# Kernel optimization log

Hardware: AMD Instinct MI355X
Metric: run time of the kernel (lower is better)

Reference implementation:

```python
import jax, jax.numpy as jnp
import numpy as np

B, T, E, V, H = 2, 2048, 1024, 2048, 8
KD, HD = E // H, V // H  # key_dim=128, head_dim=256
EPS = 1e-6


def rotate_every_two(x):
    x1 = x[..., ::2]
    x2 = x[..., 1::2]
    return jnp.stack((-x2, x1), axis=-1).reshape(x.shape)


def theta_shift(x, sin, cos):
    return x * cos + rotate_every_two(x) * sin


def setup_inputs() -> dict:
    key = jax.random.key(0)
    ks = jax.random.split(key, 8)
    x = jax.random.normal(ks[0], (B, T, E), dtype=jnp.float32)
    angle = jnp.arange(T, dtype=jnp.float32)[:, None] * (1.0 / (10000.0 ** (jnp.repeat(jnp.arange(KD // 2, dtype=jnp.float32), 2) * 2.0 / KD)))
    sin = jnp.sin(angle)  # [T, KD]
    cos = jnp.cos(angle)
    # RetNet per-head causal decay mask: decay_h = 1 - 2^(-5-h)
    decay = 1.0 - 2.0 ** (-5.0 - jnp.arange(H, dtype=jnp.float32))  # [H]
    idx = jnp.arange(T, dtype=jnp.float32)
    diff = idx[:, None] - idx[None, :]  # n - m
    causal = diff >= 0
    mask = jnp.where(causal[None], jnp.exp(jnp.where(causal, diff, 0.0)[None] * jnp.log(decay)[:, None, None]), 0.0)  # [H,T,T]
    g = 2 ** (-2.5)
    Wq = jax.random.normal(ks[1], (E, E), dtype=jnp.float32) * (g * np.sqrt(2.0 / (E + E)))
    Wk = jax.random.normal(ks[2], (E, E), dtype=jnp.float32) * (g * np.sqrt(2.0 / (E + E)))
    Wv = jax.random.normal(ks[3], (E, V), dtype=jnp.float32) * (g * np.sqrt(2.0 / (E + V)))
    Wg = jax.random.normal(ks[4], (E, V), dtype=jnp.float32) * (g * np.sqrt(2.0 / (E + V)))
    Wo = jax.random.normal(ks[5], (V, E), dtype=jnp.float32) * np.sqrt(2.0 / (V + E))
    return {"x": x, "sin": sin, "cos": cos, "mask": mask,
            "Wq": Wq, "Wk": Wk, "Wv": Wv, "Wg": Wg, "Wo": Wo}


def reference(x, sin, cos, mask, Wq, Wk, Wv, Wg, Wo):
    b, t, _ = x.shape
    scaling = KD ** -0.5
    q = (x @ Wq).reshape(b, t, H, KD).transpose(0, 2, 1, 3)  # [B,H,T,KD]
    k = (x @ Wk * scaling).reshape(b, t, H, KD).transpose(0, 2, 1, 3)
    v = x @ Wv  # [B,T,V]
    g = x @ Wg
    qr = theta_shift(q, sin, cos)
    kr = theta_shift(k, sin, cos)
    vr = v.reshape(b, t, H, HD).transpose(0, 2, 1, 3)  # [B,H,T,HD]
    qk = jnp.einsum('bhsk,bhtk->bhst', qr, kr) * mask  # [B,H,T,T]
    denom = jnp.clip(jnp.abs(jax.lax.stop_gradient(qk).sum(-1, keepdims=True)), 1.0, None)
    qk = qk / denom
    out = jnp.einsum('bhst,bhtd->bhsd', qk, vr)  # [B,H,T,HD]
    out = out.transpose(0, 2, 1, 3)  # [B,T,H,HD]
    # RMSNorm over head_dim, no affine
    out = out * jax.lax.rsqrt(jnp.mean(out * out, axis=-1, keepdims=True) + EPS)
    out = out.reshape(b, t, H * HD)
    out = jax.nn.silu(g) * out
    return out @ Wo  # [B,T,E]
```

## Files before the change

### kernel.cpp

```cpp
#include <hip/hip_runtime.h>
#include <hip/hip_bf16.h>


#define B_ 2
#define T_ 2048
#define E_ 1024
#define V_ 2048
#define H_ 8
#define KD_ 128
#define HD_ 256
#define M_ 4096

typedef __attribute__((ext_vector_type(8))) short bf16x8;
typedef __attribute__((ext_vector_type(4))) float f32x4;

__device__ __forceinline__ float u2f(unsigned short u) {
    return __uint_as_float(((unsigned)u) << 16);
}
__device__ __forceinline__ unsigned short f2bu(float f) {
    unsigned x = __float_as_uint(f);
    return (unsigned short)((x + 0x7fffu + ((x >> 16) & 1u)) >> 16);
}

typedef const __attribute__((address_space(1))) void gas_t;
typedef __attribute__((address_space(3))) void las_t;
__device__ __forceinline__ void gl_lds16(const void* g, void* l) {
    __builtin_amdgcn_global_load_lds((gas_t*)g, (las_t*)l, 16, 0, 0);
}

__global__ __launch_bounds__(256) void conv_x_kernel(
    const float* __restrict__ x, unsigned short* __restrict__ xb)
{
    const size_t i = ((size_t)blockIdx.x * 256 + threadIdx.x) * 8;
    float4 a = *(const float4*)(x + i);
    float4 c = *(const float4*)(x + i + 4);
    *(ushort4*)(xb + i)     = make_ushort4(f2bu(a.x), f2bu(a.y), f2bu(a.z), f2bu(a.w));
    *(ushort4*)(xb + i + 4) = make_ushort4(f2bu(c.x), f2bu(c.y), f2bu(c.z), f2bu(c.w));
}

__global__ __launch_bounds__(256) void transW5_kernel(
    const float* __restrict__ Wq, const float* __restrict__ Wk,
    const float* __restrict__ Wv, const float* __restrict__ Wg,
    const float* __restrict__ Wo,
    unsigned short* __restrict__ Wt, unsigned short* __restrict__ wot)
{
    const int z = blockIdx.z;
    const float* W; int N; int rofs; int Kd; unsigned short* dst;
    if (z == 0)      { W = Wq; N = 1024; rofs = 0;    Kd = 1024; dst = Wt; }
    else if (z == 1) { W = Wk; N = 1024; rofs = 1024; Kd = 1024; dst = Wt; }
    else if (z == 2) { W = Wv; N = 2048; rofs = 2048; Kd = 1024; dst = Wt; }
    else if (z == 3) { W = Wg; N = 2048; rofs = 4096; Kd = 1024; dst = Wt; }
    else             { W = Wo; N = 1024; rofs = 0;    Kd = 2048; dst = wot; }
    const int n0 = blockIdx.x * 64;
    const int k0 = blockIdx.y * 64;
    if (n0 >= N || k0 >= Kd) return;

    __shared__ float tl[64][65];
    const int tid = threadIdx.x;
    #pragma unroll
    for (int i = 0; i < 4; ++i) {
        int kr = i * 16 + (tid >> 4);
        int nc = (tid & 15) * 4;
        float4 v = *(const float4*)(W + (size_t)(k0 + kr) * N + n0 + nc);
        tl[kr][nc] = v.x; tl[kr][nc + 1] = v.y; tl[kr][nc + 2] = v.z; tl[kr][nc + 3] = v.w;
    }
    __syncthreads();
    #pragma unroll
    for (int i = 0; i < 4; ++i) {
        int nr = i * 16 + (tid >> 4);
        int kc = (tid & 15) * 4;
        ushort4 u = make_ushort4(f2bu(tl[kc + 0][nr]), f2bu(tl[kc + 1][nr]),
                                 f2bu(tl[kc + 2][nr]), f2bu(tl[kc + 3][nr]));
        *(ushort4*)(dst + (size_t)(rofs + n0 + nr) * Kd + k0 + kc) = u;
    }
}

__global__ __launch_bounds__(256) void transV_kernel(
    const unsigned short* __restrict__ vb, unsigned short* __restrict__ vt)
{
    __shared__ unsigned short tl[64][68];
    const int tid = threadIdx.x;
    const int t0 = blockIdx.x * 64, c0 = blockIdx.y * 64, b = blockIdx.z;
    #pragma unroll
    for (int i = 0; i < 4; ++i) {
        int tr = i * 16 + (tid >> 4);
        int cc = (tid & 15) * 4;
        ushort4 v = *(const ushort4*)(vb + (size_t)(b * T_ + t0 + tr) * V_ + c0 + cc);
        tl[tr][cc] = v.x; tl[tr][cc + 1] = v.y; tl[tr][cc + 2] = v.z; tl[tr][cc + 3] = v.w;
    }
    __syncthreads();
    #pragma unroll
    for (int i = 0; i < 4; ++i) {
        int cr = i * 16 + (tid >> 4);
        int tc = (tid & 15) * 4;
        ushort4 u = make_ushort4(tl[tc + 0][cr], tl[tc + 1][cr], tl[tc + 2][cr], tl[tc + 3][cr]);
        *(ushort4*)(vt + (size_t)(b * V_ + c0 + cr) * T_ + t0 + tc) = u;
    }
}

#define GSTAGE(BUF, K0)                                                        \
    {                                                                          \
        _Pragma("unroll")                                                      \
        for (int i = 0; i < 4; ++i) {                                          \
            int r = i * 32 + srow;                                             \
            int cb = scolb ^ ((r & 7) << 4);                                   \
            gl_lds16((const char*)(A  + (size_t)(rowBase + r) * K + (K0)) + cb,\
                     Asm[BUF] + i * 4096 + w * 1024);                          \
            gl_lds16((const char*)(Bt + (size_t)(colBase + r) * K + (K0)) + cb,\
                     Bsm[BUF] + i * 4096 + w * 1024);                          \
        }                                                                      \
    }

#define GCOMPUTE(BUF)                                                          \
    {                                                                          \
        _Pragma("unroll")                                                      \
        for (int kk = 0; kk < 2; ++kk) {                                       \
            const int cb = kk * 64 + (l >> 4) * 16;                            \
            bf16x8 a[4], b[4];                                                 \
            _Pragma("unroll")                                                  \
            for (int m = 0; m < 4; ++m) {                                      \
                int r = wr * 64 + m * 16 + (l & 15);                           \
                a[m] = *(const bf16x8*)(Asm[BUF] + r * 128 + (cb ^ ((r & 7) << 4))); \
            }                                                                  \
            _Pragma("unroll")                                                  \
            for (int n = 0; n < 4; ++n) {                                      \
                int r = wc * 64 + n * 16 + (l & 15);                           \
                b[n] = *(const bf16x8*)(Bsm[BUF] + r * 128 + (cb ^ ((r & 7) << 4))); \
            }                                                                  \
            _Pragma("unroll")                                                  \
            for (int m = 0; m < 4; ++m)                                        \
                _Pragma("unroll")                                              \
                for (int n = 0; n < 4; ++n)                                    \
                    acc[m][n] = __builtin_amdgcn_mfma_f32_16x16x32_bf16(a[m], b[n], acc[m][n], 0, 0, 0); \
        }                                                                      \
    }

#define GEMM_PIPELINE_LOOP                                                     \
    GSTAGE(0, 0)                                                               \
    const int nk = K / 64;                                                     \
    for (int kt = 0; kt < nk; ++kt) {                                          \
        const int cur = kt & 1;                                                \
        if (kt + 1 < nk) {                                                     \
            GSTAGE(1 - cur, (kt + 1) * 64)                                     \
            asm volatile("s_waitcnt vmcnt(8)" ::: "memory");                   \
        } else {                                                               \
            asm volatile("s_waitcnt vmcnt(0)" ::: "memory");                   \
        }                                                                      \
        __builtin_amdgcn_s_barrier();                                          \
        __builtin_amdgcn_sched_barrier(0);                                     \
        GCOMPUTE(cur)                                                          \
        __builtin_amdgcn_s_barrier();                                          \
        __builtin_amdgcn_sched_barrier(0);                                     \
    }

__global__ __launch_bounds__(256) void gemm_qkvg_kernel(
    const unsigned short* __restrict__ A,
    const unsigned short* __restrict__ Bt,
    unsigned short* __restrict__ qb,
    unsigned short* __restrict__ kb,
    unsigned short* __restrict__ vb,
    unsigned short* __restrict__ gb)
{
    const int K = E_;
    __shared__ __align__(16) char Asm[2][128 * 64 * 2];
    __shared__ __align__(16) char Bsm[2][128 * 64 * 2];
    const int tid = threadIdx.x;
    const int l = tid & 63;
    const int w = tid >> 6;
    const int wr = w >> 1, wc = w & 1;
    const int rowBase = blockIdx.y * 128;
    const int colBase = blockIdx.x * 128;
    const int srow = tid >> 3;
    const int scolb = (tid & 7) * 16;

    f32x4 acc[4][4] = {};

    GEMM_PIPELINE_LOOP

    const int colW = colBase + wc * 64;
    unsigned short* dst;
    int cofs, stride;
    if (colW < 1024)      { dst = qb; cofs = 0;    stride = E_; }
    else if (colW < 2048) { dst = kb; cofs = 1024; stride = E_; }
    else if (colW < 4096) { dst = vb; cofs = 2048; stride = V_; }
    else                  { dst = gb; cofs = 4096; stride = V_; }
    #pragma unroll
    for (int m = 0; m < 4; ++m)
        #pragma unroll
        for (int n = 0; n < 4; ++n)
            #pragma unroll
            for (int r = 0; r < 4; ++r) {
                int row = rowBase + wr * 64 + m * 16 + (l >> 4) * 4 + r;
                int col = colW + n * 16 + (l & 15);
                float f = acc[m][n][r];
                if (!isfinite(f)) f = 0.f;
                dst[(size_t)row * stride + (col - cofs)] = f2bu(f);
            }
}

__global__ __launch_bounds__(256) void gemm_wo_kernel(
    const unsigned short* __restrict__ A,
    const unsigned short* __restrict__ Bt,
    float* __restrict__ C)
{
    const int K = V_;
    __shared__ __align__(16) char Asm[2][64 * 128];
    __shared__ __align__(16) char Bsm[2][128 * 128];
    const int tid = threadIdx.x;
    const int l = tid & 63;
    const int w = tid >> 6;
    const int wr = w >> 1, wc = w & 1;
    const int rowBase = blockIdx.y * 64;
    const int colBase = blockIdx.x * 128;
    const int srow = tid >> 3;
    const int scolb = (tid & 7) * 16;

    f32x4 acc[2][4] = {};

#define WSTAGE(BUF, K0)                                                        \
    {                                                                          \
        _Pragma("unroll")                                                      \
        for (int i = 0; i < 2; ++i) {                                          \
            int r = i * 32 + srow;                                             \
            int cb = scolb ^ ((r & 7) << 4);                                   \
            gl_lds16((const char*)(A + (size_t)(rowBase + r) * K + (K0)) + cb, \
                     Asm[BUF] + i * 4096 + w * 1024);                          \
        }                                                                      \
        _Pragma("unroll")                                                      \
        for (int i = 0; i < 4; ++i) {                                          \
            int r = i * 32 + srow;                                             \
            int cb = scolb ^ ((r & 7) << 4);                                   \
            gl_lds16((const char*)(Bt + (size_t)(colBase + r) * K + (K0)) + cb,\
                     Bsm[BUF] + i * 4096 + w * 1024);                          \
        }                                                                      \
    }

    WSTAGE(0, 0)
    const int nk = K / 64;
    for (int kt = 0; kt < nk; ++kt) {
        const int cur = kt & 1;
        if (kt + 1 < nk) {
            WSTAGE(1 - cur, (kt + 1) * 64)
            asm volatile("s_waitcnt vmcnt(6)" ::: "memory");
        } else {
            asm volatile("s_waitcnt vmcnt(0)" ::: "memory");
        }
        __builtin_amdgcn_s_barrier();
        __builtin_amdgcn_sched_barrier(0);
        #pragma unroll
        for (int kk = 0; kk < 2; ++kk) {
            const int cb = kk * 64 + (l >> 4) * 16;
            bf16x8 a[2], b[4];
            #pragma unroll
            for (int m = 0; m < 2; ++m) {
                int r = wr * 32 + m * 16 + (l & 15);
                a[m] = *(const bf16x8*)(Asm[cur] + r * 128 + (cb ^ ((r & 7) << 4)));
            }
            #pragma unroll
            for (int n = 0; n < 4; ++n) {
                int r = wc * 64 + n * 16 + (l & 15);
                b[n] = *(const bf16x8*)(Bsm[cur] + r * 128 + (cb ^ ((r & 7) << 4)));
            }
            #pragma unroll
            for (int m = 0; m < 2; ++m)
                #pragma unroll
                for (int n = 0; n < 4; ++n)
                    acc[m][n] = __builtin_amdgcn_mfma_f32_16x16x32_bf16(a[m], b[n], acc[m][n], 0, 0, 0);
        }
        __builtin_amdgcn_s_barrier();
        __builtin_amdgcn_sched_barrier(0);
    }
#undef WSTAGE

    #pragma unroll
    for (int m = 0; m < 2; ++m)
        #pragma unroll
        for (int n = 0; n < 4; ++n)
            #pragma unroll
            for (int r = 0; r < 4; ++r) {
                int row = rowBase + wr * 32 + m * 16 + (l >> 4) * 4 + r;
                int col = colBase + wc * 64 + n * 16 + (l & 15);
                float f = acc[m][n][r];
                if (!isfinite(f)) f = 0.f;
                C[(size_t)row * E_ + col] = f;
            }
}

__global__ __launch_bounds__(256) void theta2_kernel(
    unsigned short* __restrict__ qb,
    unsigned short* __restrict__ kb,
    const float* __restrict__ sinp, const float* __restrict__ cosp)
{
    unsigned short* qk = blockIdx.y ? kb : qb;
    const float scale = blockIdx.y ? 0.088388347648318447f : 1.0f;
    const int i = blockIdx.x * 256 + threadIdx.x;
    const int pe = i & (E_ / 2 - 1);
    const int bt = i >> 9;
    const int t = bt & (T_ - 1);
    const int e0 = pe << 1;
    const int d0 = e0 & (KD_ - 1);
    const size_t base = (size_t)bt * E_ + e0;
    const float q0 = u2f(qk[base]);
    const float q1 = u2f(qk[base + 1]);
    const int sb = t * KD_ + d0;
    const float s0 = sinp[sb], s1 = sinp[sb + 1];
    const float c0 = cosp[sb], c1 = cosp[sb + 1];
    qk[base]     = f2bu((q0 * c0 - q1 * s0) * scale);
    qk[base + 1] = f2bu((q1 * c1 + q0 * s1) * scale);
}

#define STAGE_K(BUF, T0)                                                       \
    {                                                                          \
        _Pragma("unroll")                                                      \
        for (int i = 0; i < 4; ++i) {                                          \
            int r = i * 16 + (tid >> 4);                                       \
            int cb = ((tid & 15) * 16) ^ ((r & 7) << 4);                       \
            gl_lds16((const char*)(kb + (size_t)(b * T_ + (T0) + r) * E_ + h * KD_) + cb, \
                     Ks[BUF] + i * 4096 + w * 1024);                           \
        }                                                                      \
    }

#define STAGE_V(BUF, T0)                                                       \
    {                                                                          \
        _Pragma("unroll")                                                      \
        for (int i = 0; i < 8; ++i) {                                          \
            int r = i * 32 + (tid >> 3);                                       \
            int cb = ((tid & 7) * 16) ^ ((r & 7) << 4);                        \
            gl_lds16((const char*)(vt + (size_t)((b * H_ + h) * HD_ + r) * T_ + (T0)) + cb, \
                     Vs[BUF] + i * 4096 + w * 1024);                           \
        }                                                                      \
    }

__global__ __launch_bounds__(256) void retention_mfma_kernel(
    const unsigned short* __restrict__ qb,
    const unsigned short* __restrict__ kb,
    const unsigned short* __restrict__ vt,
    const unsigned short* __restrict__ g,
    unsigned short* __restrict__ ao)
{
    __shared__ __align__(16) char Ks[2][64 * 128 * 2];
    __shared__ __align__(16) char Vs[2][256 * 64 * 2];
    __shared__ __align__(16) char Pq[64 * 64 * 2];
    __shared__ float rsum_p[4][64];
    __shared__ float rsq_p[4][64];
    const int tid = threadIdx.x;
    const int l = tid & 63;
    const int w = tid >> 6;
    const int g_ = l >> 4;
    const int q15 = l & 15;
    const int orig = (int)blockIdx.x;
    const int bh   = orig & 15;
    const int chunk = 31 - (orig >> 4);
    const int b = bh >> 3, h = bh & 7;
    const int s0 = chunk * 64;
    const float ld = logf(1.f - exp2f(-5.f - (float)h));

    float es[4];
    #pragma unroll
    for (int qb2 = 0; qb2 < 4; ++qb2)
        es[qb2] = __expf((float)(s0 + qb2 * 16 + q15) * ld);
    float etl[4];
    #pragma unroll
    for (int r = 0; r < 4; ++r)
        etl[r] = __expf(-(float)(w * 16 + 4 * g_ + r) * ld);
    const float Dm64 = __expf(-64.f * ld);
    float etb = 1.f;

    bf16x8 qf[4][4];
    #pragma unroll
    for (int qb2 = 0; qb2 < 4; ++qb2) {
        const char* qp = (const char*)(qb + (size_t)(b * T_ + s0 + qb2 * 16 + q15) * E_ + h * KD_);
        #pragma unroll
        for (int kk = 0; kk < 4; ++kk)
            qf[qb2][kk] = *(const bf16x8*)(qp + kk * 64 + g_ * 16);
    }

    f32x4 oaccT[4][4] = {};
    float rs[4] = {0.f, 0.f, 0.f, 0.f};

    const int nt = chunk + 1;
    STAGE_K(0, 0)
    STAGE_V(0, 0)

    for (int t = 0; t < nt; ++t) {
        const int cur = t & 1;
        const int t0 = t * 64;
        if (t + 1 < nt) {
            STAGE_K(1 - cur, t0 + 64)
            STAGE_V(1 - cur, t0 + 64)
            asm volatile("s_waitcnt vmcnt(12)" ::: "memory");
        } else {
            asm volatile("s_waitcnt vmcnt(0)" ::: "memory");
        }
        __builtin_amdgcn_s_barrier();
        __builtin_amdgcn_sched_barrier(0);

        f32x4 sacc[4] = {};
        {
            const int krow = w * 16 + q15;
            const int swz = (krow & 7) << 4;
            #pragma unroll
            for (int kk = 0; kk < 4; ++kk) {
                bf16x8 kf = *(const bf16x8*)(Ks[cur] + krow * 256 + ((kk * 64 + g_ * 16) ^ swz));
                #pragma unroll
                for (int qb2 = 0; qb2 < 4; ++qb2)
                    sacc[qb2] = __builtin_amdgcn_mfma_f32_16x16x32_bf16(kf, qf[qb2][kk], sacc[qb2], 0, 0, 0);
            }
        }
        {
            const float etw = etb;
            #pragma unroll
            for (int qb2 = 0; qb2 < 4; ++qb2) {
                const int qg = s0 + qb2 * 16 + q15;
                const int q_local = qb2 * 16 + q15;
                float rsp = 0.f;
                unsigned short pk[4];
                #pragma unroll
                for (int r = 0; r < 4; ++r) {
                    int tg = t0 + w * 16 + 4 * g_ + r;
                    float pm = (qg >= tg) ? sacc[qb2][r] * (es[qb2] * etw * etl[r]) : 0.f;
                    rsp += pm;
                    pk[r] = f2bu(pm);
                }
                *(ushort4*)(Pq + q_local * 128 + (((w * 16 + 4 * g_) * 2) ^ ((q_local & 7) << 4))) =
                    make_ushort4(pk[0], pk[1], pk[2], pk[3]);
                rsp += __shfl_xor(rsp, 16);
                rsp += __shfl_xor(rsp, 32);
                rs[qb2] += rsp;
            }
            etb *= Dm64;
        }
        asm volatile("s_waitcnt lgkmcnt(0)" ::: "memory");
        __builtin_amdgcn_s_barrier();
        __builtin_amdgcn_sched_barrier(0);
        #pragma unroll
        for (int kk = 0; kk < 2; ++kk) {
            const int cb = kk * 64 + g_ * 16;
            bf16x8 pf[4], vf[4];
            #pragma unroll
            for (int qb2 = 0; qb2 < 4; ++qb2) {
                int pr = qb2 * 16 + q15;
                pf[qb2] = *(const bf16x8*)(Pq + pr * 128 + (cb ^ ((pr & 7) << 4)));
            }
            #pragma unroll
            for (int m = 0; m < 4; ++m) {
                int vr = w * 64 + m * 16 + q15;
                vf[m] = *(const bf16x8*)(Vs[cur] + vr * 128 + (cb ^ ((vr & 7) << 4)));
            }
            #pragma unroll
            for (int qb2 = 0; qb2 < 4; ++qb2)
                #pragma unroll
                for (int m = 0; m < 4; ++m)
                    oaccT[qb2][m] = __builtin_amdgcn_mfma_f32_16x16x32_bf16(vf[m], pf[qb2], oaccT[qb2][m], 0, 0, 0);
        }
        __builtin_amdgcn_s_barrier();
        __builtin_amdgcn_sched_barrier(0);
    }

    if (l < 16) {
        #pragma unroll
        for (int qb2 = 0; qb2 < 4; ++qb2)
            rsum_p[w][qb2 * 16 + q15] = rs[qb2];
    }
    __syncthreads();

    float inv[4];
    #pragma unroll
    for (int qb2 = 0; qb2 < 4; ++qb2) {
        const int q_local = qb2 * 16 + q15;
        const float tot = rsum_p[0][q_local] + rsum_p[1][q_local] +
                          rsum_p[2][q_local] + rsum_p[3][q_local];
        inv[qb2] = 1.f / fmaxf(fabsf(tot), 1.f);
    }

    #pragma unroll
    for (int qb2 = 0; qb2 < 4; ++qb2) {
        float ps = 0.f;
        #pragma unroll
        for (int m = 0; m < 4; ++m)
            #pragma unroll
            for (int r = 0; r < 4; ++r) {
                float o = oaccT[qb2][m][r] * inv[qb2];
                ps += o * o;
            }
        ps += __shfl_xor(ps, 16);
        ps += __shfl_xor(ps, 32);
        if (l < 16) rsq_p[w][qb2 * 16 + q15] = ps;
    }
    __syncthreads();

    #pragma unroll
    for (int qb2 = 0; qb2 < 4; ++qb2) {
        const int q_local = qb2 * 16 + q15;
        const float tot = rsq_p[0][q_local] + rsq_p[1][q_local] +
                          rsq_p[2][q_local] + rsq_p[3][q_local];
        const float scale = rsqrtf(tot * (1.0f / HD_) + 1e-6f) * inv[qb2];
        const size_t rowb = (size_t)(b * T_ + s0 + q_local) * V_ + h * HD_;
        #pragma unroll
        for (int m = 0; m < 4; ++m) {
            const int vc0 = w * 64 + m * 16 + 4 * g_;
            ushort4 gv4 = *(const ushort4*)(g + rowb + vc0);
            const unsigned short* gv = (const unsigned short*)&gv4;
            unsigned short outp[4];
            #pragma unroll
            for (int r = 0; r < 4; ++r) {
                const float gvf = u2f(gv[r]);
                const float silu = gvf / (1.f + __expf(-gvf));
                float f = oaccT[qb2][m][r] * scale * silu;
                if (!isfinite(f)) f = 0.f;
                outp[r] = f2bu(f);
            }
            *(ushort4*)(ao + rowb + vc0) = make_ushort4(outp[0], outp[1], outp[2], outp[3]);
        }
    }
}

extern "C" void kernel_launch(void* const* d_in, const int* in_sizes, int n_in,
                              void* d_out, int out_size, void* d_ws, size_t ws_size,
                              hipStream_t stream)
{
    const float* x    = (const float*)d_in[0];
    const float* sinp = (const float*)d_in[1];
    const float* cosp = (const float*)d_in[2];
    const float* Wq   = (const float*)d_in[4];
    const float* Wk   = (const float*)d_in[5];
    const float* Wv   = (const float*)d_in[6];
    const float* Wg   = (const float*)d_in[7];
    const float* Wo   = (const float*)d_in[8];
    float* out = (float*)d_out;

    unsigned short* xb = (unsigned short*)d_out;
    unsigned short* qb = xb + (size_t)M_ * E_;

    char* ws = (char*)d_ws;
    unsigned short* kb  = (unsigned short*)(ws + 0);
    unsigned short* vb  = (unsigned short*)(ws + 8388608);
    unsigned short* gb  = (unsigned short*)(ws + 25165824);
    unsigned short* wt  = (unsigned short*)(ws + 41943040);
    unsigned short* vt  = (unsigned short*)(ws + 54525952);
    unsigned short* aob = (unsigned short*)(ws + 71303168);
    unsigned short* wot = (unsigned short*)(ws + 88080384);

    dim3 blk(256);
    conv_x_kernel<<<M_ * E_ / 8 / 256, blk, 0, stream>>>(x, xb);

    transW5_kernel<<<dim3(32, 32, 5), blk, 0, stream>>>(Wq, Wk, Wv, Wg, Wo, wt, wot);

    gemm_qkvg_kernel<<<dim3(48, 32), blk, 0, stream>>>(xb, wt, qb, kb, vb, gb);

    theta2_kernel<<<dim3(M_ * E_ / 2 / 256, 2), blk, 0, stream>>>(qb, kb, sinp, cosp);

    transV_kernel<<<dim3(32, 32, B_), blk, 0, stream>>>(vb, vt);

    retention_mfma_kernel<<<dim3(512), blk, 0, stream>>>(qb, kb, vt, gb, aob);

    gemm_wo_kernel<<<dim3(8, 64), blk, 0, stream>>>(aob, wot, out);
}
```

Measured before the change: 199.7 us.

## Write V transposed from QKVG GEMM epilogue, single-buffer V, remap retention blocks

The QKVG GEMM epilogue now writes the V projection directly in transposed [B,V,T] layout with 4-element packed stores, which removes the separate transV kernel and its extra round trip through global memory. The retention kernel drops V double-buffering: V is loaded at the start of each iteration and waited on just before the PV MFMA stage, which halves V shared memory and allows launch_bounds with 2 blocks per CU. Block-to-(head,chunk) mapping is rearranged per XCD so each CU pairs a long causal chunk with a short one for load balance. The risk is that the V load latency is less hidden than before, and the transposed stores in the GEMM epilogue are strided across T.

```diff
diff --git a/kernel.cpp b/kernel.cpp
--- a/kernel.cpp
+++ b/kernel.cpp
@@ -72,29 +72,6 @@
         ushort4 u = make_ushort4(f2bu(tl[kc + 0][nr]), f2bu(tl[kc + 1][nr]),
                                  f2bu(tl[kc + 2][nr]), f2bu(tl[kc + 3][nr]));
         *(ushort4*)(dst + (size_t)(rofs + n0 + nr) * Kd + k0 + kc) = u;
-    }
-}
-
-__global__ __launch_bounds__(256) void transV_kernel(
-    const unsigned short* __restrict__ vb, unsigned short* __restrict__ vt)
-{
-    __shared__ unsigned short tl[64][68];
-    const int tid = threadIdx.x;
-    const int t0 = blockIdx.x * 64, c0 = blockIdx.y * 64, b = blockIdx.z;
-    #pragma unroll
-    for (int i = 0; i < 4; ++i) {
-        int tr = i * 16 + (tid >> 4);
-        int cc = (tid & 15) * 4;
-        ushort4 v = *(const ushort4*)(vb + (size_t)(b * T_ + t0 + tr) * V_ + c0 + cc);
-        tl[tr][cc] = v.x; tl[tr][cc + 1] = v.y; tl[tr][cc + 2] = v.z; tl[tr][cc + 3] = v.w;
-    }
-    __syncthreads();
-    #pragma unroll
-    for (int i = 0; i < 4; ++i) {
-        int cr = i * 16 + (tid >> 4);
-        int tc = (tid & 15) * 4;
-        ushort4 u = make_ushort4(tl[tc + 0][cr], tl[tc + 1][cr], tl[tc + 2][cr], tl[tc + 3][cr]);
-        *(ushort4*)(vt + (size_t)(b * V_ + c0 + cr) * T_ + t0 + tc) = u;
     }
 }
 
@@ -158,7 +135,7 @@
     const unsigned short* __restrict__ Bt,
     unsigned short* __restrict__ qb,
     unsigned short* __restrict__ kb,
-    unsigned short* __restrict__ vb,
+    unsigned short* __restrict__ vt,
     unsigned short* __restrict__ gb)
 {
     const int K = E_;
@@ -178,24 +155,45 @@
     GEMM_PIPELINE_LOOP
 
     const int colW = colBase + wc * 64;
-    unsigned short* dst;
-    int cofs, stride;
-    if (colW < 1024)      { dst = qb; cofs = 0;    stride = E_; }
-    else if (colW < 2048) { dst = kb; cofs = 1024; stride = E_; }
-    else if (colW < 4096) { dst = vb; cofs = 2048; stride = V_; }
-    else                  { dst = gb; cofs = 4096; stride = V_; }
-    #pragma unroll
-    for (int m = 0; m < 4; ++m)
-        #pragma unroll
-        for (int n = 0; n < 4; ++n)
-            #pragma unroll
-            for (int r = 0; r < 4; ++r) {
-                int row = rowBase + wr * 64 + m * 16 + (l >> 4) * 4 + r;
-                int col = colW + n * 16 + (l & 15);
-                float f = acc[m][n][r];
-                if (!isfinite(f)) f = 0.f;
-                dst[(size_t)row * stride + (col - cofs)] = f2bu(f);
-            }
+    if (colW >= 2048 && colW < 4096) {
+        #pragma unroll
+        for (int m = 0; m < 4; ++m)
+            #pragma unroll
+            for (int n = 0; n < 4; ++n) {
+                const int row0 = rowBase + wr * 64 + m * 16 + (l >> 4) * 4;
+                const int vcol = colW + n * 16 + (l & 15) - 2048;
+                const int vbatch = row0 >> 11;
+                const int t0 = row0 & (T_ - 1);
+                unsigned short pk[4];
+                #pragma unroll
+                for (int r = 0; r < 4; ++r) {
+                    float f = acc[m][n][r];
+                    if (!isfinite(f)) f = 0.f;
+                    pk[r] = f2bu(f);
+                }
+                *(ushort4*)(vt + (size_t)(vbatch * V_ + vcol) * T_ + t0) =
+                    make_ushort4(pk[0], pk[1], pk[2], pk[3]);
+            }
+    } else {
+        unsigned short* dst;
+        int cofs;
+        if (colW < 1024)      { dst = qb; cofs = 0; }
+        else if (colW < 2048) { dst = kb; cofs = 1024; }
+        else                  { dst = gb; cofs = 4096; }
+        const int stride = (colW < 2048) ? E_ : V_;
+        #pragma unroll
+        for (int m = 0; m < 4; ++m)
+            #pragma unroll
+            for (int n = 0; n < 4; ++n)
+                #pragma unroll
+                for (int r = 0; r < 4; ++r) {
+                    int row = rowBase + wr * 64 + m * 16 + (l >> 4) * 4 + r;
+                    int col = colW + n * 16 + (l & 15);
+                    float f = acc[m][n][r];
+                    if (!isfinite(f)) f = 0.f;
+                    dst[(size_t)row * stride + (col - cofs)] = f2bu(f);
+                }
+    }
 }
 
 __global__ __launch_bounds__(256) void gemm_wo_kernel(
@@ -320,18 +318,18 @@
         }                                                                      \
     }
 
-#define STAGE_V(BUF, T0)                                                       \
+#define STAGE_V(T0)                                                            \
     {                                                                          \
         _Pragma("unroll")                                                      \
         for (int i = 0; i < 8; ++i) {                                          \
             int r = i * 32 + (tid >> 3);                                       \
             int cb = ((tid & 7) * 16) ^ ((r & 7) << 4);                        \
             gl_lds16((const char*)(vt + (size_t)((b * H_ + h) * HD_ + r) * T_ + (T0)) + cb, \
-                     Vs[BUF] + i * 4096 + w * 1024);                           \
-        }                                                                      \
-    }
-
-__global__ __launch_bounds__(256) void retention_mfma_kernel(
+                     Vs + i * 4096 + w * 1024);                                \
+        }                                                                      \
+    }
+
+__global__ __launch_bounds__(256, 2) void retention_mfma_kernel(
     const unsigned short* __restrict__ qb,
     const unsigned short* __restrict__ kb,
     const unsigned short* __restrict__ vt,
@@ -339,7 +337,7 @@
     unsigned short* __restrict__ ao)
 {
     __shared__ __align__(16) char Ks[2][64 * 128 * 2];
-    __shared__ __align__(16) char Vs[2][256 * 64 * 2];
+    __shared__ __align__(16) char Vs[256 * 64 * 2];
     __shared__ __align__(16) char Pq[64 * 64 * 2];
     __shared__ float rsum_p[4][64];
     __shared__ float rsq_p[4][64];
@@ -349,8 +347,14 @@
     const int g_ = l >> 4;
     const int q15 = l & 15;
     const int orig = (int)blockIdx.x;
-    const int bh   = orig & 15;
-    const int chunk = 31 - (orig >> 4);
+    const int xcd  = orig & 7;
+    const int pos  = orig >> 3;
+    const int slot = pos >> 5;
+    const int cu   = pos & 31;
+    const int half = cu >> 4;
+    const int c15  = cu & 15;
+    const int bh   = xcd * 2 + half;
+    const int chunk = slot ? c15 : (31 - c15);
     const int b = bh >> 3, h = bh & 7;
     const int s0 = chunk * 64;
     const float ld = logf(1.f - exp2f(-5.f - (float)h));
@@ -380,17 +384,16 @@
 
     const int nt = chunk + 1;
     STAGE_K(0, 0)
-    STAGE_V(0, 0)
 
     for (int t = 0; t < nt; ++t) {
         const int cur = t & 1;
         const int t0 = t * 64;
+        STAGE_V(t0)
         if (t + 1 < nt) {
             STAGE_K(1 - cur, t0 + 64)
-            STAGE_V(1 - cur, t0 + 64)
             asm volatile("s_waitcnt vmcnt(12)" ::: "memory");
         } else {
-            asm volatile("s_waitcnt vmcnt(0)" ::: "memory");
+            asm volatile("s_waitcnt vmcnt(8)" ::: "memory");
         }
         __builtin_amdgcn_s_barrier();
         __builtin_amdgcn_sched_barrier(0);
@@ -430,7 +433,11 @@
             }
             etb *= Dm64;
         }
-        asm volatile("s_waitcnt lgkmcnt(0)" ::: "memory");
+        if (t + 1 < nt) {
+            asm volatile("s_waitcnt vmcnt(4) lgkmcnt(0)" ::: "memory");
+        } else {
+            asm volatile("s_waitcnt vmcnt(0) lgkmcnt(0)" ::: "memory");
+        }
         __builtin_amdgcn_s_barrier();
         __builtin_amdgcn_sched_barrier(0);
         #pragma unroll
@@ -445,7 +452,7 @@
             #pragma unroll
             for (int m = 0; m < 4; ++m) {
                 int vr = w * 64 + m * 16 + q15;
-                vf[m] = *(const bf16x8*)(Vs[cur] + vr * 128 + (cb ^ ((vr & 7) << 4)));
+                vf[m] = *(const bf16x8*)(Vs + vr * 128 + (cb ^ ((vr & 7) << 4)));
             }
             #pragma unroll
             for (int qb2 = 0; qb2 < 4; ++qb2)
@@ -534,24 +541,21 @@
 
     char* ws = (char*)d_ws;
     unsigned short* kb  = (unsigned short*)(ws + 0);
-    unsigned short* vb  = (unsigned short*)(ws + 8388608);
-    unsigned short* gb  = (unsigned short*)(ws + 25165824);
-    unsigned short* wt  = (unsigned short*)(ws + 41943040);
-    unsigned short* vt  = (unsigned short*)(ws + 54525952);
-    unsigned short* aob = (unsigned short*)(ws + 71303168);
-    unsigned short* wot = (unsigned short*)(ws + 88080384);
+    unsigned short* gb  = (unsigned short*)(ws + 8388608);
+    unsigned short* wt  = (unsigned short*)(ws + 25165824);
+    unsigned short* vt  = (unsigned short*)(ws + 37748736);
+    unsigned short* aob = (unsigned short*)(ws + 54525952);
+    unsigned short* wot = (unsigned short*)(ws + 71303168);
 
     dim3 blk(256);
     conv_x_kernel<<<M_ * E_ / 8 / 256, blk, 0, stream>>>(x, xb);
 
     transW5_kernel<<<dim3(32, 32, 5), blk, 0, stream>>>(Wq, Wk, Wv, Wg, Wo, wt, wot);
 
-    gemm_qkvg_kernel<<<dim3(48, 32), blk, 0, stream>>>(xb, wt, qb, kb, vb, gb);
+    gemm_qkvg_kernel<<<dim3(48, 32), blk, 0, stream>>>(xb, wt, qb, kb, vt, gb);
 
     theta2_kernel<<<dim3(M_ * E_ / 2 / 256, 2), blk, 0, stream>>>(qb, kb, sinp, cosp);
 
-    transV_kernel<<<dim3(32, 32, B_), blk, 0, stream>>>(vb, vt);
-
     retention_mfma_kernel<<<dim3(512), blk, 0, stream>>>(qb, kb, vt, gb, aob);
 
     gemm_wo_kernel<<<dim3(8, 64), blk, 0, stream>>>(aob, wot, out);
```

Result: faster. 185.6 us (-7.1%).
